# Kernel optimization log

Hardware: AMD Instinct MI355X
Metric: run time of the kernel (lower is better)

## Reference

```python
import jax, jax.numpy as jnp
import numpy as np

SIZE = 896
HALF = SIZE // 2
BINS = 256  # 2 ** (16 / 2)


def _scale(idx):
    # map bin index [0, BINS-1] -> [-1, 1]
    return idx.astype(jnp.float32) / ((BINS - 1) / 2.0) - 1.0


def setup_inputs() -> dict:
    key = jax.random.key(0)
    ks = jax.random.split(key, 13)
    B, T = 32, 256
    rn = lambda k, shape, s: jax.random.normal(k, shape, dtype=jnp.float32) * s
    return {
        "conditional": rn(ks[0], (B, T, 3, SIZE), 0.1),
        "hidden_state": rn(ks[1], (B, SIZE), 0.1),
        "gru_input_bias": rn(ks[2], (3 * SIZE,), 0.1),
        "gru_hidden_weight": rn(ks[3], (3 * SIZE, SIZE), 0.05),
        "gru_hidden_bias": rn(ks[4], (3 * SIZE,), 0.1),
        "w_coarse_in": rn(ks[5], (3 * HALF, 2), 0.5),
        "b_coarse_in": rn(ks[6], (3 * HALF,), 0.1),
        "w_fine_in": rn(ks[7], (3 * HALF, 3), 0.5),
        "b_fine_in": rn(ks[8], (3 * HALF,), 0.1),
        "w_bins_coarse": rn(ks[9], (BINS, HALF), 0.05),
        "b_bins_coarse": rn(ks[10], (BINS,), 0.1),
        "w_bins_fine": rn(ks[11], (BINS, HALF), 0.05),
        "b_bins_fine": rn(ks[12], (BINS,), 0.1),
    }


def reference(conditional, hidden_state, gru_input_bias, gru_hidden_weight,
              gru_hidden_bias, w_coarse_in, b_coarse_in, w_fine_in, b_fine_in,
              w_bins_coarse, b_bins_coarse, w_bins_fine, b_bins_fine):
    B = conditional.shape[0]
    # add GRU input biases per gate (r, u, e)
    cond = conditional + gru_input_bias.reshape(3, SIZE)  # [B,T,3,SIZE]
    # split each gate into coarse/fine halves and regroup: [B,T,3*HALF]
    cond_c = jnp.concatenate([cond[:, :, 0, :HALF], cond[:, :, 1, :HALF], cond[:, :, 2, :HALF]], axis=-1)
    cond_f = jnp.concatenate([cond[:, :, 0, HALF:], cond[:, :, 1, HALF:], cond[:, :, 2, HALF:]], axis=-1)
    cond_c = jnp.swapaxes(cond_c, 0, 1)  # [T,B,3*HALF] time-major for scan
    cond_f = jnp.swapaxes(cond_f, 0, 1)

    # initial go-sample: split_signal(0) -> coarse bin 128, fine bin 0
    coarse0 = jnp.full((B, 1), 128.0 / 127.5 - 1.0, dtype=jnp.float32)
    fine0 = jnp.full((B, 1), -1.0, dtype=jnp.float32)
    ch0 = hidden_state[:, :HALF]
    fh0 = hidden_state[:, HALF:]

    def step(carry, x):
        coarse, fine, ch, fh = carry
        xc, xf = x
        hp = jnp.concatenate([ch, fh], axis=1) @ gru_hidden_weight.T + gru_hidden_bias  # [B,3*SIZE]
        hcr, hfr, hcu, hfu, hce, hfe = jnp.split(hp, 6, axis=1)  # each [B,HALF]
        # ---- coarse half-GRU ----
        ci = jnp.concatenate([coarse, fine], axis=1)  # [B,2]
        cp = ci @ w_coarse_in.T + b_coarse_in + xc  # [B,3*HALF]
        ru = jax.nn.sigmoid(cp[:, :SIZE] + jnp.concatenate([hcr, hcu], axis=1))
        r, u = ru[:, :HALF], ru[:, HALF:]
        e = jnp.tanh(r * hce + cp[:, SIZE:])
        ch = u * ch + (1.0 - u) * e
        c_idx = jnp.argmax(ch @ w_bins_coarse.T + b_bins_coarse, axis=1)  # [B]
        coarse = _scale(c_idx)[:, None]
        # ---- fine half-GRU ----
        fi = jnp.concatenate([ci, coarse], axis=1)  # [B,3]
        fp = fi @ w_fine_in.T + b_fine_in + xf
        ru = jax.nn.sigmoid(fp[:, :SIZE] + jnp.concatenate([hfr, hfu], axis=1))
        r, u = ru[:, :HALF], ru[:, HALF:]
        e = jnp.tanh(r * hfe + fp[:, SIZE:])
        fh = u * fh + (1.0 - u) * e
        f_idx = jnp.argmax(fh @ w_bins_fine.T + b_bins_fine, axis=1)
        fine = _scale(f_idx)[:, None]
        return (coarse, fine, ch, fh), (c_idx, f_idx)

    (_, _, ch, fh), (oc, of) = jax.lax.scan(step, (coarse0, fine0, ch0, fh0), (cond_c, cond_f))
    hidden = jnp.concatenate([ch, fh], axis=1)  # [B,SIZE]
    return jnp.swapaxes(oc, 0, 1), jnp.swapaxes(of, 0, 1), hidden
```

## Files before the change

### kernel.cpp

```cpp
#include <hip/hip_runtime.h>

#define NWG  56
#define NBLK 57
#define NTHR 384
#define TT   256
#define SPLITF   2048.0f
#define INVSPLIT 4.8828125e-4f

typedef _Float16 f16;
typedef __attribute__((ext_vector_type(8))) _Float16 f16x8;
typedef __attribute__((ext_vector_type(4))) float f32x4;

__device__ __forceinline__ float sigacc(float x){ return 1.0f/(1.0f + expf(-x)); }

__device__ __forceinline__ unsigned long long amax_key(float v, int bin, unsigned tag){
  unsigned u = __float_as_uint(v);
  u = (u & 0x80000000u) ? ~u : (u | 0x80000000u);
  return ((unsigned long long)u << 32) | ((unsigned long long)(tag & 0xFFFFu) << 8)
       | (unsigned)(255 - bin);
}

__device__ __forceinline__ int grp_base(int g){ return 448 * ((g < 3) ? (2*g) : (2*g - 5)); }

__device__ __forceinline__ void xchg32(unsigned* p, unsigned v){
  __hip_atomic_exchange(p, v, __ATOMIC_RELAXED, __HIP_MEMORY_SCOPE_AGENT);
}
__device__ __forceinline__ void xchg64(unsigned long long* p, unsigned long long v){
  __hip_atomic_exchange(p, v, __ATOMIC_RELAXED, __HIP_MEMORY_SCOPE_AGENT);
}
__device__ __forceinline__ unsigned ldg32(const unsigned* p){
  return __hip_atomic_load(p, __ATOMIC_RELAXED, __HIP_MEMORY_SCOPE_AGENT);
}
__device__ __forceinline__ unsigned long long ldg64(const void* p){
  return __hip_atomic_load((const unsigned long long*)p, __ATOMIC_RELAXED, __HIP_MEMORY_SCOPE_AGENT);
}
__device__ __forceinline__ void drain(){ asm volatile("s_waitcnt vmcnt(0)" ::: "memory"); }
__device__ __forceinline__ int f16bits(f16 h){
  return (int)__builtin_bit_cast(unsigned short, h);
}

__global__ void pack_gru(const float* __restrict__ W, f16* __restrict__ outH, f16* __restrict__ outL){
  int blk = blockIdx.x;
  int ks  = blk % 14;
  int rest= blk / 14;
  int wv  = rest % 6, w = rest / 6;
  int mt  = wv >> 1, kh = wv & 1;
  int l   = threadIdx.x;
  int lr  = mt*16 + (l & 15);
  int R   = grp_base(lr >> 3) + 8*w + (lr & 7);
  int k   = kh*448 + ks*32 + (l >> 4)*8;
  const float* src = W + (size_t)R*896 + k;
  f16x8 vh, vl;
  #pragma unroll
  for (int i=0;i<8;i++){
    float x = src[i];
    f16 h = (f16)x;
    vh[i] = h;
    vl[i] = (f16)((x - (float)h) * SPLITF);
  }
  size_t o = (size_t)blk*64 + l;
  ((f16x8*)outH)[o] = vh;
  ((f16x8*)outL)[o] = vl;
}

__global__ void pack_bins(const float* __restrict__ Wc, const float* __restrict__ Wf,
                          f16* __restrict__ oCh, f16* __restrict__ oCl,
                          f16* __restrict__ oFh, f16* __restrict__ oFl){
  int blk  = blockIdx.x;
  int half = blk / 224;
  int rem  = blk % 224;
  int ks   = rem % 14, wg = rem / 14;
  int l    = threadIdx.x;
  const float* W = half ? Wf : Wc;
  f16* oh = half ? oFh : oCh;
  f16* ol = half ? oFl : oCl;
  int bin = wg*16 + (l & 15);
  int k   = ks*32 + (l >> 4)*8;
  const float* src = W + (size_t)bin*448 + k;
  f16x8 vh, vl;
  #pragma unroll
  for (int i=0;i<8;i++){
    float x = src[i];
    f16 h = (f16)x;
    vh[i] = h;
    vl[i] = (f16)((x - (float)h) * SPLITF);
  }
  size_t o = (size_t)rem*64 + l;
  ((f16x8*)oh)[o] = vh;
  ((f16x8*)ol)[o] = vl;
}

__launch_bounds__(NTHR, 1)
__global__ void wavernn_main(
    const float* __restrict__ cond,
    const float* __restrict__ h0,
    const float* __restrict__ gib,
    const float* __restrict__ ghb,
    const float* __restrict__ wci,
    const float* __restrict__ bci,
    const float* __restrict__ wfi,
    const float* __restrict__ bfi,
    const float* __restrict__ bbc,
    const float* __restrict__ bbf,
    const f16*  __restrict__ wsAh, const f16* __restrict__ wsAl,
    const f16*  __restrict__ wsBCh, const f16* __restrict__ wsBCl,
    const f16*  __restrict__ wsBFh, const f16* __restrict__ wsBFl,
    unsigned*   __restrict__ Hg,
    unsigned long long* __restrict__ partC,
    unsigned long long* __restrict__ partF,
    unsigned*   __restrict__ flags,
    unsigned*   __restrict__ resC,
    unsigned*   __restrict__ resF,
    float* __restrict__ out)
{
  __shared__ float hpL[48][33];
  __shared__ float coarseL[32], fineL[32];
  __shared__ f16x8 binBh0[896], binBl0[896], binBh1[896], binBl1[896];
  __shared__ float wclL[3][8][2], bclL[3][8], wflL[3][8][3], bflL[3][8], hblL[48];

  const int w   = blockIdx.x;
  const int tid = threadIdx.x;
  const int wv  = tid >> 6;
  const int l   = tid & 63;

  auto poll_parts = [&](const unsigned long long* part, unsigned tgt)->unsigned long long {
    int bb = l & 31;
    unsigned long long k0,k1,k2,k3,k4,k5,k6,k7,k8,k9,k10,k11,k12,k13,k14,k15;
    for(;;){
      k0=ldg64(&part[0*32+bb]);  k1=ldg64(&part[1*32+bb]);
      k2=ldg64(&part[2*32+bb]);  k3=ldg64(&part[3*32+bb]);
      k4=ldg64(&part[4*32+bb]);  k5=ldg64(&part[5*32+bb]);
      k6=ldg64(&part[6*32+bb]);  k7=ldg64(&part[7*32+bb]);
      k8=ldg64(&part[8*32+bb]);  k9=ldg64(&part[9*32+bb]);
      k10=ldg64(&part[10*32+bb]); k11=ldg64(&part[11*32+bb]);
      k12=ldg64(&part[12*32+bb]); k13=ldg64(&part[13*32+bb]);
      k14=ldg64(&part[14*32+bb]); k15=ldg64(&part[15*32+bb]);
      unsigned long long tmask = 0xFFFF00ull, texp = (unsigned long long)tgt << 8;
      bool ok = ((k0&tmask)==texp) & ((k1&tmask)==texp) & ((k2&tmask)==texp) & ((k3&tmask)==texp)
              & ((k4&tmask)==texp) & ((k5&tmask)==texp) & ((k6&tmask)==texp) & ((k7&tmask)==texp)
              & ((k8&tmask)==texp) & ((k9&tmask)==texp) & ((k10&tmask)==texp)& ((k11&tmask)==texp)
              & ((k12&tmask)==texp)& ((k13&tmask)==texp)& ((k14&tmask)==texp)& ((k15&tmask)==texp);
      if (__all(ok)) break;
      __builtin_amdgcn_s_sleep(1);
    }
    unsigned long long m01=k0>k1?k0:k1, m23=k2>k3?k2:k3, m45=k4>k5?k4:k5, m67=k6>k7?k6:k7;
    unsigned long long m89=k8>k9?k8:k9, mab=k10>k11?k10:k11, mcd=k12>k13?k12:k13, mef=k14>k15?k14:k15;
    unsigned long long a=m01>m23?m01:m23, c=m45>m67?m45:m67, d=m89>mab?m89:mab, f=mcd>mef?mcd:mef;
    unsigned long long x=a>c?a:c, y=d>f?d:f;
    return x>y?x:y;
  };

  if (w == NWG) {
    if (wv == 0) {
      for (int t=0; t<TT; t++){
        unsigned tgt = (unsigned)(t+1);
        unsigned long long best = poll_parts(partC, tgt);
        int bin = 255 - (int)(best & 0xFFull);
        if (l < 32) {
          out[l*TT + t] = (float)bin;
          xchg32(&resC[l], (tgt << 16) | (unsigned)bin);
        }
      }
    } else if (wv == 1) {
      for (int t=0; t<TT; t++){
        unsigned tgt = (unsigned)(t+1);
        unsigned long long best = poll_parts(partF, tgt);
        int bin = 255 - (int)(best & 0xFFull);
        if (l < 32) {
          out[8192 + l*TT + t] = (float)bin;
          xchg32(&resF[l], (tgt << 16) | (unsigned)bin);
        }
      }
    }
    return;
  }

  const int mt  = wv >> 1, kh = wv & 1;
  const int b   = tid >> 3, e = tid & 7;
  const bool owner = tid < 256;
  const int jc  = 8*w + e;

  unsigned* fE0 = flags;
  unsigned* fE1 = flags + 64;
  unsigned* fE3 = flags + 128;

  f16x8 afh[14], afl[14];
  {
    const f16x8* Ah = (const f16x8*)wsAh + (size_t)(w*6 + wv)*14*64;
    const f16x8* Al = (const f16x8*)wsAl + (size_t)(w*6 + wv)*14*64;
    #pragma unroll
    for (int ks=0; ks<14; ks++){ afh[ks] = Ah[ks*64 + l]; afl[ks] = Al[ks*64 + l]; }
  }
  if (w < 16) {
    const f16x8* s0 = (const f16x8*)wsBCh + (size_t)w*896;
    const f16x8* s1 = (const f16x8*)wsBCl + (size_t)w*896;
    const f16x8* s2 = (const f16x8*)wsBFh + (size_t)w*896;
    const f16x8* s3 = (const f16x8*)wsBFl + (size_t)w*896;
    for (int i = tid; i < 896; i += NTHR) {
      binBh0[i] = s0[i]; binBl0[i] = s1[i];
      binBh1[i] = s2[i]; binBl1[i] = s3[i];
    }
  }
  if (tid < 48) hblL[tid] = ghb[grp_base(tid>>3) + 8*w + (tid&7)];
  if (tid < 24) {
    int p = tid >> 3, ee = tid & 7;
    int j = p*448 + 8*w + ee;
    wclL[p][ee][0] = wci[j*2+0]; wclL[p][ee][1] = wci[j*2+1];
    bclL[p][ee]    = bci[j] + gib[p*896 + 8*w + ee];
    wflL[p][ee][0] = wfi[j*3+0]; wflL[p][ee][1] = wfi[j*3+1]; wflL[p][ee][2] = wfi[j*3+2];
    bflL[p][ee]    = bfi[j] + gib[p*896 + 448 + 8*w + ee];
  }
  if (tid < 32) { coarseL[tid] = 128.0f/127.5f - 1.0f; fineL[tid] = -1.0f; }
  float biasC = 0.f, biasF = 0.f;
  if (w < 16) { biasC = bbc[w*16 + (l&15)]; biasF = bbf[w*16 + (l&15)]; }

  auto store_half = [&](unsigned* Hrow, int fine, float val){
    f16 hh = (f16)val;
    f16 hl = (f16)((val - (float)hh) * SPLITF);
    int pk = f16bits(hh) | (f16bits(hl) << 16);
    int nb = __shfl_down(pk, 1);
    if (!(e & 1)) {
      int off = fine*224 + (jc >> 1);
      unsigned hi32 = (unsigned)((pk & 0xffff) | (nb << 16));
      unsigned lo32 = ((unsigned)pk >> 16) | ((unsigned)nb & 0xffff0000u);
      xchg32(Hrow + off,       hi32);
      xchg32(Hrow + 448 + off, lo32);
    }
  };

  auto wait56 = [&](const unsigned* f, int n, unsigned tgt){
    const unsigned* p = f + ((l < n) ? l : 0);
    for(;;){
      unsigned v = ldg32(p);
      if (__all(v == tgt)) break;
      __builtin_amdgcn_s_sleep(1);
    }
    unsigned vv = __hip_atomic_load(p, __ATOMIC_ACQUIRE, __HIP_MEMORY_SCOPE_AGENT);
    asm volatile("" :: "v"(vv) : "memory");
  };
  auto poll_res = [&](const unsigned* res, unsigned tgt)->int{
    const unsigned* p = res + (l & 31);
    unsigned v;
    for(;;){
      v = ldg32(p);
      if (__all((v >> 16) == tgt)) break;
      __builtin_amdgcn_s_sleep(1);
    }
    asm volatile("" ::: "memory");
    return (int)(v & 0xFFFFu);
  };

  float chS = 0.f, fhS = 0.f;
  if (owner) {
    chS = h0[b*896 + jc];
    fhS = h0[b*896 + 448 + jc];
    unsigned* Hrow = Hg + b*896;
    store_half(Hrow, 0, chS);
    store_half(Hrow, 1, fhS);
  }
  drain();
  __syncthreads();
  if (tid == 0) xchg32(&fE0[w], 1u);
  if (wv == 0) wait56(fE0, 56, 1u);
  __syncthreads();

  float xcr=0, xcu=0, xce=0, xfr=0, xfu=0, xfe=0;
  auto prefetch = [&](int t){
    if (owner) {
      const float* cb_ = cond + ((size_t)b*TT + t)*2688;
      xcr = cb_[jc];        xcu = cb_[896 + jc];  xce = cb_[1792 + jc];
      xfr = cb_[448 + jc];  xfu = cb_[1344 + jc]; xfe = cb_[2240 + jc];
    }
  };
  auto do_gemm = [&](const unsigned* H){
    f32x4 ah0={0,0,0,0}, al0={0,0,0,0}, ah1={0,0,0,0}, al1={0,0,0,0};
    const f16* base0 = (const f16*)(H + (size_t)(l&15)*896 + kh*224 + (l>>4)*4);
    const f16* base1 = (const f16*)(H + (size_t)((l&15)+16)*896 + kh*224 + (l>>4)*4);
    #pragma unroll
    for (int ks=0; ks<14; ks++) {
      f16x8 bh0 = *(const f16x8*)(base0 + ks*32);
      f16x8 bl0 = *(const f16x8*)(base0 + 896 + ks*32);
      f16x8 bh1 = *(const f16x8*)(base1 + ks*32);
      f16x8 bl1 = *(const f16x8*)(base1 + 896 + ks*32);
      ah0 = __builtin_amdgcn_mfma_f32_16x16x32_f16(afh[ks], bh0, ah0, 0,0,0);
      al0 = __builtin_amdgcn_mfma_f32_16x16x32_f16(afh[ks], bl0, al0, 0,0,0);
      al0 = __builtin_amdgcn_mfma_f32_16x16x32_f16(afl[ks], bh0, al0, 0,0,0);
      ah1 = __builtin_amdgcn_mfma_f32_16x16x32_f16(afh[ks], bh1, ah1, 0,0,0);
      al1 = __builtin_amdgcn_mfma_f32_16x16x32_f16(afh[ks], bl1, al1, 0,0,0);
      al1 = __builtin_amdgcn_mfma_f32_16x16x32_f16(afl[ks], bh1, al1, 0,0,0);
    }
    if (kh == 0) {
      #pragma unroll
      for (int i=0;i<4;i++){
        int row = mt*16 + (l>>4)*4 + i;
        hpL[row][l&15]      = ah0[i] + al0[i]*INVSPLIT + hblL[row];
        hpL[row][16+(l&15)] = ah1[i] + al1[i]*INVSPLIT + hblL[row];
      }
    }
    __syncthreads();
    if (kh == 1) {
      #pragma unroll
      for (int i=0;i<4;i++){
        int row = mt*16 + (l>>4)*4 + i;
        hpL[row][l&15]      += ah0[i] + al0[i]*INVSPLIT;
        hpL[row][16+(l&15)] += ah1[i] + al1[i]*INVSPLIT;
      }
    }
    __syncthreads();
  };
  auto do_bins = [&](const unsigned* H, int fine, const f16x8* Bh, const f16x8* Bl,
                     float bias, unsigned long long* part, unsigned tgt){
    f32x4 acch={0,0,0,0}, accl={0,0,0,0};
    const f16* ar = (const f16*)(H + (size_t)(wv*16 + (l&15))*896 + fine*224 + (l>>4)*4);
    #pragma unroll
    for (int ks=0; ks<14; ks++) {
      f16x8 ah  = *(const f16x8*)(ar + ks*32);
      f16x8 al_ = *(const f16x8*)(ar + 896 + ks*32);
      f16x8 bh = Bh[ks*64 + l];
      f16x8 bl = Bl[ks*64 + l];
      acch = __builtin_amdgcn_mfma_f32_16x16x32_f16(ah,  bh, acch, 0,0,0);
      accl = __builtin_amdgcn_mfma_f32_16x16x32_f16(ah,  bl, accl, 0,0,0);
      accl = __builtin_amdgcn_mfma_f32_16x16x32_f16(al_, bh, accl, 0,0,0);
    }
    #pragma unroll
    for (int i=0;i<4;i++){
      unsigned long long key = amax_key(acch[i] + accl[i]*INVSPLIT + bias, w*16 + (l&15), tgt);
      #pragma unroll
      for (int m=1; m<16; m<<=1){
        unsigned long long o = __shfl_xor(key, m, 16);
        key = (o > key) ? o : key;
      }
      if ((l&15)==0) xchg64(&part[w*32 + wv*16 + (l>>4)*4 + i], key);
    }
  };

  prefetch(0);
  do_gemm(Hg);

  for (int t=0; t<TT; t++) {
    unsigned* Hn = Hg + (((t+1)&1) ? 28672 : 0);
    const unsigned tgt = (unsigned)(t+1);

    float cprev = 0.f, fprev = 0.f;
    if (owner) {
      cprev = coarseL[b]; fprev = fineL[b];
      float cpr = cprev*wclL[0][e][0] + fprev*wclL[0][e][1] + bclL[0][e] + xcr;
      float cpu_= cprev*wclL[1][e][0] + fprev*wclL[1][e][1] + bclL[1][e] + xcu;
      float cpe = cprev*wclL[2][e][0] + fprev*wclL[2][e][1] + bclL[2][e] + xce;
      float r  = sigacc(cpr  + hpL[e][b]);
      float u  = sigacc(cpu_ + hpL[8+e][b]);
      float g  = tanhf(fmaf(r, hpL[16+e][b], cpe));
      chS = fmaf(u, chS - g, g);
      store_half(Hn + b*896, 0, chS);
    }
    drain();
    __syncthreads();
    if (tid == 0) xchg32(&fE1[w], tgt);

    if (w < 16) {
      if (wv == 0) wait56(fE1, 56, tgt);
      __syncthreads();
      if (wv < 2) do_bins(Hn, 0, binBh0, binBl0, biasC, partC, tgt);
    }
    if (wv == 0) {
      int bin = poll_res(resC, tgt);
      if (l < 32) coarseL[l] = (float)bin * (1.0f/127.5f) - 1.0f;
    }
    __syncthreads();

    if (owner) {
      float cnew = coarseL[b];
      float fpr = cprev*wflL[0][e][0] + fprev*wflL[0][e][1] + cnew*wflL[0][e][2] + bflL[0][e] + xfr;
      float fpu = cprev*wflL[1][e][0] + fprev*wflL[1][e][1] + cnew*wflL[1][e][2] + bflL[1][e] + xfu;
      float fpe = cprev*wflL[2][e][0] + fprev*wflL[2][e][1] + cnew*wflL[2][e][2] + bflL[2][e] + xfe;
      float r  = sigacc(fpr + hpL[24+e][b]);
      float u  = sigacc(fpu + hpL[32+e][b]);
      float g  = tanhf(fmaf(r, hpL[40+e][b], fpe));
      fhS = fmaf(u, fhS - g, g);
      store_half(Hn + b*896, 1, fhS);
    }
    drain();
    __syncthreads();
    if (tid == 0) xchg32(&fE3[w], tgt);

    if (w < 16) {
      if (wv == 0) wait56(fE3, 56, tgt);
      __syncthreads();
      if (wv < 2) do_bins(Hn, 1, binBh1, binBl1, biasF, partF, tgt);
    }

    if (t < TT-1) {
      prefetch(t+1);
      if (w >= 16) {
        if (wv == 0) wait56(fE3, 56, tgt);
        __syncthreads();
      }
      do_gemm(Hn);
    }

    if (wv == 0) {
      int bin = poll_res(resF, tgt);
      if (l < 32) fineL[l] = (float)bin * (1.0f/127.5f) - 1.0f;
    }
    __syncthreads();
  }

  if (owner) {
    out[16384 + b*896 + jc]        = chS;
    out[16384 + b*896 + 448 + jc]  = fhS;
  }
}

#define WS_AH    0u
#define WS_AL    4816896u
#define WS_BCH   9633792u
#define WS_BCL   9863168u
#define WS_BFH   10092544u
#define WS_BFL   10321920u
#define WS_HG    10551296u
#define WS_FLAGS 10780672u
#define WS_PC    10781696u
#define WS_PF    10785792u
#define WS_RES   10789888u

extern "C" void kernel_launch(void* const* d_in, const int* in_sizes, int n_in,
                              void* d_out, int out_size, void* d_ws, size_t ws_size,
                              hipStream_t stream) {
  const float* conditional = (const float*)d_in[0];
  const float* hidden0     = (const float*)d_in[1];
  const float* gib         = (const float*)d_in[2];
  const float* ghw         = (const float*)d_in[3];
  const float* ghb         = (const float*)d_in[4];
  const float* wci         = (const float*)d_in[5];
  const float* bci         = (const float*)d_in[6];
  const float* wfi         = (const float*)d_in[7];
  const float* bfi         = (const float*)d_in[8];
  const float* wbc         = (const float*)d_in[9];
  const float* bbc         = (const float*)d_in[10];
  const float* wbf         = (const float*)d_in[11];
  const float* bbf         = (const float*)d_in[12];

  char* ws = (char*)d_ws;
  f16* wsAh  = (f16*)(ws + WS_AH);
  f16* wsAl  = (f16*)(ws + WS_AL);
  f16* wsBCh = (f16*)(ws + WS_BCH);
  f16* wsBCl = (f16*)(ws + WS_BCL);
  f16* wsBFh = (f16*)(ws + WS_BFH);
  f16* wsBFl = (f16*)(ws + WS_BFL);
  unsigned* Hg = (unsigned*)(ws + WS_HG);
  unsigned* flags = (unsigned*)(ws + WS_FLAGS);
  unsigned long long* partC = (unsigned long long*)(ws + WS_PC);
  unsigned long long* partF = (unsigned long long*)(ws + WS_PF);
  unsigned* resC = (unsigned*)(ws + WS_RES);
  unsigned* resF = (unsigned*)(ws + WS_RES + 128);
  float* out = (float*)d_out;

  hipMemsetAsync(ws + WS_FLAGS, 0, 16384, stream);
  pack_gru<<<dim3(56*6*14), dim3(64), 0, stream>>>(ghw, wsAh, wsAl);
  pack_bins<<<dim3(448), dim3(64), 0, stream>>>(wbc, wbf, wsBCh, wsBCl, wsBFh, wsBFl);
  wavernn_main<<<dim3(NBLK), dim3(NTHR), 0, stream>>>(
      conditional, hidden0, gib, ghb, wci, bci, wfi, bfi, bbc, bbf,
      wsAh, wsAl, wsBCh, wsBCl, wsBFh, wsBFl,
      Hg, partC, partF, flags, resC, resF, out);
}
```

Measured before the change: 5.675 ms.

## Split hidden GEMM into K-halves overlapped with coarse and fine bin phases

Waves are remapped so three waves own the first K-half of the hidden-state GEMM and three own the second. The first half now runs while the coarse bins are computed and the coarse result is awaited, and the second half runs alongside the fine bins. Polling moves to waves that do not run bins, so the serial GEMM step at the end of each timestep drops off the critical path. Fine-gate hidden preactivations are read into registers early so hpL can be overwritten by the next step's GEMM. The risk is subtle hpL read/write ordering and extra load on the MFMA units during the latency-critical bin phases.

```diff
diff --git a/kernel.cpp b/kernel.cpp
--- a/kernel.cpp
+++ b/kernel.cpp
@@ -145,8 +145,8 @@
     }
     unsigned long long m01=k0>k1?k0:k1, m23=k2>k3?k2:k3, m45=k4>k5?k4:k5, m67=k6>k7?k6:k7;
     unsigned long long m89=k8>k9?k8:k9, mab=k10>k11?k10:k11, mcd=k12>k13?k12:k13, mef=k14>k15?k14:k15;
-    unsigned long long a=m01>m23?m01:m23, c=m45>m67?m45:m67, d=m89>mab?m89:mab, f=mcd>mef?mcd:mef;
-    unsigned long long x=a>c?a:c, y=d>f?d:f;
+    unsigned long long a=m01>m23?m01:m23, c2=m45>m67?m45:m67, d=m89>mab?m89:mab, f=mcd>mef?mcd:mef;
+    unsigned long long x=a>c2?a:c2, y=d>f?d:f;
     return x>y?x:y;
   };
 
@@ -175,7 +175,6 @@
     return;
   }
 
-  const int mt  = wv >> 1, kh = wv & 1;
   const int b   = tid >> 3, e = tid & 7;
   const bool owner = tid < 256;
   const int jc  = 8*w + e;
@@ -184,10 +183,13 @@
   unsigned* fE1 = flags + 64;
   unsigned* fE3 = flags + 128;
 
+  const int g_kh = (wv >= 2 && wv <= 4) ? 0 : 1;
+  const int g_mt = (wv >= 2 && wv <= 4) ? (wv - 2) : (wv == 5 ? 2 : wv);
+
   f16x8 afh[14], afl[14];
   {
-    const f16x8* Ah = (const f16x8*)wsAh + (size_t)(w*6 + wv)*14*64;
-    const f16x8* Al = (const f16x8*)wsAl + (size_t)(w*6 + wv)*14*64;
+    const f16x8* Ah = (const f16x8*)wsAh + (size_t)(w*6 + (g_mt*2 + g_kh))*14*64;
+    const f16x8* Al = (const f16x8*)wsAl + (size_t)(w*6 + (g_mt*2 + g_kh))*14*64;
     #pragma unroll
     for (int ks=0; ks<14; ks++){ afh[ks] = Ah[ks*64 + l]; afl[ks] = Al[ks*64 + l]; }
   }
@@ -272,10 +274,10 @@
       xfr = cb_[448 + jc];  xfu = cb_[1344 + jc]; xfe = cb_[2240 + jc];
     }
   };
-  auto do_gemm = [&](const unsigned* H){
+  auto gemm_half = [&](const unsigned* H, bool add){
     f32x4 ah0={0,0,0,0}, al0={0,0,0,0}, ah1={0,0,0,0}, al1={0,0,0,0};
-    const f16* base0 = (const f16*)(H + (size_t)(l&15)*896 + kh*224 + (l>>4)*4);
-    const f16* base1 = (const f16*)(H + (size_t)((l&15)+16)*896 + kh*224 + (l>>4)*4);
+    const f16* base0 = (const f16*)(H + (size_t)(l&15)*896 + g_kh*224 + (l>>4)*4);
+    const f16* base1 = (const f16*)(H + (size_t)((l&15)+16)*896 + g_kh*224 + (l>>4)*4);
     #pragma unroll
     for (int ks=0; ks<14; ks++) {
       f16x8 bh0 = *(const f16x8*)(base0 + ks*32);
@@ -289,29 +291,24 @@
       al1 = __builtin_amdgcn_mfma_f32_16x16x32_f16(afh[ks], bl1, al1, 0,0,0);
       al1 = __builtin_amdgcn_mfma_f32_16x16x32_f16(afl[ks], bh1, al1, 0,0,0);
     }
-    if (kh == 0) {
-      #pragma unroll
-      for (int i=0;i<4;i++){
-        int row = mt*16 + (l>>4)*4 + i;
-        hpL[row][l&15]      = ah0[i] + al0[i]*INVSPLIT + hblL[row];
-        hpL[row][16+(l&15)] = ah1[i] + al1[i]*INVSPLIT + hblL[row];
+    #pragma unroll
+    for (int i=0;i<4;i++){
+      int row = g_mt*16 + (l>>4)*4 + i;
+      float v0 = ah0[i] + al0[i]*INVSPLIT;
+      float v1 = ah1[i] + al1[i]*INVSPLIT;
+      if (!add) {
+        hpL[row][l&15]      = v0 + hblL[row];
+        hpL[row][16+(l&15)] = v1 + hblL[row];
+      } else {
+        hpL[row][l&15]      += v0;
+        hpL[row][16+(l&15)] += v1;
       }
     }
-    __syncthreads();
-    if (kh == 1) {
-      #pragma unroll
-      for (int i=0;i<4;i++){
-        int row = mt*16 + (l>>4)*4 + i;
-        hpL[row][l&15]      += ah0[i] + al0[i]*INVSPLIT;
-        hpL[row][16+(l&15)] += ah1[i] + al1[i]*INVSPLIT;
-      }
-    }
-    __syncthreads();
   };
   auto do_bins = [&](const unsigned* H, int fine, const f16x8* Bh, const f16x8* Bl,
-                     float bias, unsigned long long* part, unsigned tgt){
+                     float bias, unsigned long long* part, unsigned tgt, int ntb){
     f32x4 acch={0,0,0,0}, accl={0,0,0,0};
-    const f16* ar = (const f16*)(H + (size_t)(wv*16 + (l&15))*896 + fine*224 + (l>>4)*4);
+    const f16* ar = (const f16*)(H + (size_t)(ntb*16 + (l&15))*896 + fine*224 + (l>>4)*4);
     #pragma unroll
     for (int ks=0; ks<14; ks++) {
       f16x8 ah  = *(const f16x8*)(ar + ks*32);
@@ -330,18 +327,21 @@
         unsigned long long o = __shfl_xor(key, m, 16);
         key = (o > key) ? o : key;
       }
-      if ((l&15)==0) xchg64(&part[w*32 + wv*16 + (l>>4)*4 + i], key);
+      if ((l&15)==0) xchg64(&part[w*32 + ntb*16 + (l>>4)*4 + i], key);
     }
   };
 
   prefetch(0);
-  do_gemm(Hg);
+  if (g_kh == 0) gemm_half(Hg, false);
+  __syncthreads();
+  if (g_kh == 1) gemm_half(Hg, true);
+  __syncthreads();
 
   for (int t=0; t<TT; t++) {
     unsigned* Hn = Hg + (((t+1)&1) ? 28672 : 0);
     const unsigned tgt = (unsigned)(t+1);
 
-    float cprev = 0.f, fprev = 0.f;
+    float cprev = 0.f, fprev = 0.f, hfr_ = 0.f, hfu_ = 0.f, hfe_ = 0.f;
     if (owner) {
       cprev = coarseL[b]; fprev = fineL[b];
       float cpr = cprev*wclL[0][e][0] + fprev*wclL[0][e][1] + bclL[0][e] + xcr;
@@ -350,19 +350,19 @@
       float r  = sigacc(cpr  + hpL[e][b]);
       float u  = sigacc(cpu_ + hpL[8+e][b]);
       float g  = tanhf(fmaf(r, hpL[16+e][b], cpe));
+      hfr_ = hpL[24+e][b]; hfu_ = hpL[32+e][b]; hfe_ = hpL[40+e][b];
       chS = fmaf(u, chS - g, g);
       store_half(Hn + b*896, 0, chS);
     }
     drain();
     __syncthreads();
     if (tid == 0) xchg32(&fE1[w], tgt);
-
-    if (w < 16) {
-      if (wv == 0) wait56(fE1, 56, tgt);
-      __syncthreads();
-      if (wv < 2) do_bins(Hn, 0, binBh0, binBl0, biasC, partC, tgt);
-    }
-    if (wv == 0) {
+    if (wv == 0) wait56(fE1, 56, tgt);
+    __syncthreads();
+
+    if (w < 16 && wv < 2) do_bins(Hn, 0, binBh0, binBl0, biasC, partC, tgt, wv);
+    if (g_kh == 0) gemm_half(Hn, false);
+    if (wv == 5) {
       int bin = poll_res(resC, tgt);
       if (l < 32) coarseL[l] = (float)bin * (1.0f/127.5f) - 1.0f;
     }
@@ -373,32 +373,22 @@
       float fpr = cprev*wflL[0][e][0] + fprev*wflL[0][e][1] + cnew*wflL[0][e][2] + bflL[0][e] + xfr;
       float fpu = cprev*wflL[1][e][0] + fprev*wflL[1][e][1] + cnew*wflL[1][e][2] + bflL[1][e] + xfu;
       float fpe = cprev*wflL[2][e][0] + fprev*wflL[2][e][1] + cnew*wflL[2][e][2] + bflL[2][e] + xfe;
-      float r  = sigacc(fpr + hpL[24+e][b]);
-      float u  = sigacc(fpu + hpL[32+e][b]);
-      float g  = tanhf(fmaf(r, hpL[40+e][b], fpe));
+      float r  = sigacc(fpr + hfr_);
+      float u  = sigacc(fpu + hfu_);
+      float g  = tanhf(fmaf(r, hfe_, fpe));
       fhS = fmaf(u, fhS - g, g);
       store_half(Hn + b*896, 1, fhS);
     }
     drain();
     __syncthreads();
     if (tid == 0) xchg32(&fE3[w], tgt);
-
-    if (w < 16) {
-      if (wv == 0) wait56(fE3, 56, tgt);
-      __syncthreads();
-      if (wv < 2) do_bins(Hn, 1, binBh1, binBl1, biasF, partF, tgt);
-    }
-
-    if (t < TT-1) {
-      prefetch(t+1);
-      if (w >= 16) {
-        if (wv == 0) wait56(fE3, 56, tgt);
-        __syncthreads();
-      }
-      do_gemm(Hn);
-    }
-
-    if (wv == 0) {
+    if (t < TT-1) prefetch(t+1);
+    if (wv == 0) wait56(fE3, 56, tgt);
+    __syncthreads();
+
+    if (w < 16 && (wv == 2 || wv == 3)) do_bins(Hn, 1, binBh1, binBl1, biasF, partF, tgt, wv-2);
+    if (g_kh == 1) gemm_half(Hn, true);
+    if (wv == 4) {
       int bin = poll_res(resF, tgt);
       if (l < 32) fineL[l] = (float)bin * (1.0f/127.5f) - 1.0f;
     }
```

Result: slower. 5.903 ms (+4.0%).
